# Kernel optimization log

Hardware: AMD Instinct MI355X
Metric: run time of the kernel (lower is better)

The kernel has to match this reference:

```python
import jax, jax.numpy as jnp
import numpy as np

NUM_EXPERTS = 8
TOP_K = 2
HIDDEN = 2048
INTER = 5632
NUM_TOKENS = 8192


def setup_inputs() -> dict:
    key = jax.random.key(0)
    ks = jax.random.split(key, 5)
    s_h = 1.0 / np.sqrt(HIDDEN)
    s_i = 1.0 / np.sqrt(INTER)
    return {
        "hidden_states": jax.random.normal(ks[0], (NUM_TOKENS, HIDDEN), jnp.float32),
        # router: ReplicatedLinear(hidden, num_experts, bias=False) -> weight [E, H]
        "w_router": jax.random.normal(ks[1], (NUM_EXPERTS, HIDDEN), jnp.float32) * s_h,
        # FusedMoE SiLU-gated MLP per expert: gate/up [E, H, I], down [E, I, H]
        "w_gate": jax.random.normal(ks[2], (NUM_EXPERTS, HIDDEN, INTER), jnp.float32) * s_h,
        "w_up": jax.random.normal(ks[3], (NUM_EXPERTS, HIDDEN, INTER), jnp.float32) * s_h,
        "w_down": jax.random.normal(ks[4], (NUM_EXPERTS, INTER, HIDDEN), jnp.float32) * s_i,
    }


def reference(hidden_states, w_router, w_gate, w_up, w_down):
    x = hidden_states  # [T, H]
    # Router linear (no bias)
    router_logits = x @ w_router.T  # [T, E]
    # FusedMoE topk: softmax over all experts, take top-k, renormalize=False
    probs = jax.nn.softmax(router_logits.astype(jnp.float32), axis=-1)
    topk_w, topk_idx = jax.lax.top_k(probs, TOP_K)  # [T, k]
    topk_w = topk_w.astype(x.dtype)

    out = jnp.zeros_like(x)
    for e in range(NUM_EXPERTS):
        # combine weight for tokens that routed to expert e (0 otherwise)
        w_e = jnp.sum(jnp.where(topk_idx == e, topk_w, 0.0), axis=-1)  # [T]
        h = jax.nn.silu(x @ w_gate[e]) * (x @ w_up[e])  # [T, I]
        out = out + (h @ w_down[e]) * w_e[:, None]
    return out
```

## Files before the change

### kernel.cpp

```cpp
#include <hip/hip_runtime.h>
#include <hip/hip_bf16.h>
#include <cstdint>

#define NTOK 8192
#define NEXP 8
#define HID  2048
#define INTR 5632
#define NT1  44
#define NT2  16
#define MT_MAX 32

#define XB_OFF 1048576u
#define WG_OFF 34603008u
#define WBYTES 184549376u
#define WU_OFF (WG_OFF + WBYTES)
#define WD_OFF (WU_OFF + WBYTES)
#define H_OFF  (WD_OFF + WBYTES)

typedef float f32x4  __attribute__((ext_vector_type(4)));
typedef short s16x8  __attribute__((ext_vector_type(8)));
typedef short s16x4  __attribute__((ext_vector_type(4)));

__device__ __forceinline__ short bfc(float f) {
  __hip_bfloat16 h = __float2bfloat16(f);
  return __builtin_bit_cast(short, h);
}
__device__ __forceinline__ s16x4 pk4(float4 a) {
  s16x4 v; v[0]=bfc(a.x); v[1]=bfc(a.y); v[2]=bfc(a.z); v[3]=bfc(a.w);
  return v;
}
__device__ __forceinline__ void gload16(const void* g, void* l) {
  __builtin_amdgcn_global_load_lds((const __attribute__((address_space(1))) void*)g,
                                   (__attribute__((address_space(3))) void*)l, 16, 0, 0);
}

#define DSR128(dst, addr, IMM) \
  asm volatile("ds_read_b128 %0, %1 offset:" IMM : "=v"(dst) : "v"(addr))
#define WAITLGKM(N) do { \
  asm volatile("s_waitcnt lgkmcnt(" #N ")" ::: "memory"); \
  __builtin_amdgcn_sched_barrier(0); } while (0)
#define WAITVM(N) do { \
  asm volatile("s_waitcnt vmcnt(" #N ")" ::: "memory"); \
  __builtin_amdgcn_sched_barrier(0); } while (0)

#define MFMA_BF16 __builtin_amdgcn_mfma_f32_16x16x32_bf16

__global__ __launch_bounds__(256, 4) void prep_kernel(
    const float* __restrict__ src, short* __restrict__ dst,
    int KT, int NP, int Nsrc) {
  __shared__ float tile[32 * 132];
  const int b = blockIdx.x;
  const int np = b % NP;
  const int kt = (b / NP) % KT;
  const int e  = b / (NP * KT);
  const int tid = threadIdx.x;
  const float* s = src + (size_t)e * KT * 32 * (size_t)Nsrc + (size_t)kt * 32 * Nsrc + np * 128;
#pragma unroll
  for (int i = 0; i < 4; i++) {
    const int idx = tid + i * 256;
    const int row = idx >> 5, c4 = idx & 31;
    float4 v = *(const float4*)(s + (size_t)row * Nsrc + c4 * 4);
    *(float4*)(tile + row * 132 + c4 * 4) = v;
  }
  __syncthreads();
  short* dbase = dst + ((size_t)(e * KT + kt) * (NP * 8) + np * 8) * 512;
#pragma unroll
  for (int i = 0; i < 2; i++) {
    const int c = tid + i * 256;
    const int lane = c & 63;
    const int nf = c >> 6;
    const int n = nf * 16 + (lane & 15);
    const int kb = (lane >> 4) * 8;
    s16x8 o;
#pragma unroll
    for (int j = 0; j < 8; j++) o[j] = bfc(tile[(kb + j) * 132 + n]);
    *(s16x8*)(dbase + (size_t)c * 8) = o;
  }
}

__global__ void router_kernel(const float* __restrict__ x, const float* __restrict__ wr,
                              int* __restrict__ cnt, int* __restrict__ lists,
                              float* __restrict__ wlists, __hip_bfloat16* __restrict__ xb) {
  const int wave = threadIdx.x >> 6;
  const int lane = threadIdx.x & 63;
  const int t = blockIdx.x * 4 + wave;
  if (t >= NTOK) return;
  float acc[NEXP];
#pragma unroll
  for (int e = 0; e < NEXP; e++) acc[e] = 0.f;
  const float* xrow = x + (size_t)t * HID;
  short* xbs = (short*)xb + (size_t)t * HID;
#pragma unroll
  for (int j = 0; j < HID / 256; j++) {
    const int k = j * 256 + lane * 4;
    float4 xv = *(const float4*)(xrow + k);
    *(s16x4*)(xbs + k) = pk4(xv);
#pragma unroll
    for (int e = 0; e < NEXP; e++) {
      float4 wv = *(const float4*)(wr + e * HID + k);
      acc[e] += xv.x * wv.x + xv.y * wv.y + xv.z * wv.z + xv.w * wv.w;
    }
  }
#pragma unroll
  for (int e = 0; e < NEXP; e++) {
    float v = acc[e];
    for (int off = 32; off; off >>= 1) v += __shfl_xor(v, off, 64);
    acc[e] = v;
  }
  if (lane == 0) {
    float m = acc[0];
#pragma unroll
    for (int e = 1; e < NEXP; e++) m = fmaxf(m, acc[e]);
    float p[NEXP], s = 0.f;
#pragma unroll
    for (int e = 0; e < NEXP; e++) { p[e] = __expf(acc[e] - m); s += p[e]; }
    const float inv = 1.f / s;
    int e1 = 0; float b1 = p[0];
#pragma unroll
    for (int e = 1; e < NEXP; e++) if (p[e] > b1) { b1 = p[e]; e1 = e; }
    int e2 = -1; float b2 = -1.f;
#pragma unroll
    for (int e = 0; e < NEXP; e++) if (e != e1 && p[e] > b2) { b2 = p[e]; e2 = e; }
    const int pos1 = atomicAdd(&cnt[e1], 1);
    lists[e1 * NTOK + pos1] = t; wlists[e1 * NTOK + pos1] = b1 * inv;
    const int pos2 = atomicAdd(&cnt[e2], 1);
    lists[e2 * NTOK + pos2] = t; wlists[e2 * NTOK + pos2] = b2 * inv;
  }
}

__global__ void offsets_kernel(const int* __restrict__ cnt, int* __restrict__ offs) {
  if (threadIdx.x == 0 && blockIdx.x == 0) {
    int o = 0;
#pragma unroll
    for (int e = 0; e < NEXP; e++) { offs[e] = o; o += cnt[e]; }
    offs[NEXP] = o;
  }
}

__global__ __launch_bounds__(512, 1) void gemm1_kernel(
    const __hip_bfloat16* __restrict__ xb, const short* __restrict__ wgb,
    const short* __restrict__ wub, const int* __restrict__ cnt,
    const int* __restrict__ offs, const int* __restrict__ lists,
    __hip_bfloat16* __restrict__ hbuf) {
  const int P = blockIdx.x;
  const int xcd = P & 7, slot = P >> 3;
  const int mt = slot & 31, jj = slot >> 5;
  const int g = jj * 8 + xcd;
  const int e = g / NT1, nt = g % NT1;
  const int count = cnt[e];
  if (mt * 256 >= count) return;
  const int n0 = nt * 128;
  const int lim = count - mt * 256;
  const int tid = threadIdx.x;
  const int w = tid >> 6, lane = tid & 63;
  const int wm = w >> 1, wn = w & 1;

  __shared__ short Lds[3 * 16384];
  short* rootA = &Lds[0];
  const uint32_t ldsbase = (uint32_t)(uintptr_t)rootA;

  const int* tl = lists + e * NTOK + mt * 256;
  const short* xbs = (const short*)xb;
  const short* srcA0; const short* srcA1;
  {
    const int r0 = (w * 2 + 0) * 16 + (lane & 15);
    const int r1 = (w * 2 + 1) * 16 + (lane & 15);
    const int t0 = tl[r0 < lim ? r0 : 0];
    const int t1 = tl[r1 < lim ? r1 : 0];
    srcA0 = xbs + (size_t)t0 * HID + (lane >> 4) * 8;
    srcA1 = xbs + (size_t)t1 * HID + (lane >> 4) * 8;
  }
  const short* srcBg = wgb + ((size_t)(e * 64) * 352 + nt * 8) * 512 + tid * 8;
  const short* srcBu = wub + ((size_t)(e * 64) * 352 + nt * 8) * 512 + tid * 8;

  const uint32_t roA = wm * 4096 + lane * 16;
  const uint32_t roB = 16384 + wn * 4096 + lane * 16;
  const uint32_t roU = 24576 + wn * 4096 + lane * 16;

  f32x4 accG[4][4], accU[4][4];
#pragma unroll
  for (int i = 0; i < 4; i++)
#pragma unroll
    for (int j = 0; j < 4; j++) {
      accG[i][j] = f32x4{0.f, 0.f, 0.f, 0.f};
      accU[i][j] = f32x4{0.f, 0.f, 0.f, 0.f};
    }

  uint32_t b0 = 0, b1 = 32768, b2 = 65536;

#define STG1(BOFF) do {                                                         \
    short* d = rootA + ((BOFF) >> 1);                                           \
    gload16(srcA0, d + (w * 2 + 0) * 512);                                      \
    gload16(srcA1, d + (w * 2 + 1) * 512);                                      \
    gload16(srcBg, d + 8192 + w * 512);                                         \
    gload16(srcBu, d + 12288 + w * 512);                                        \
    srcA0 += 32; srcA1 += 32; srcBg += 180224; srcBu += 180224; } while (0)

#define MMQ(NF)                                                                 \
  { __builtin_amdgcn_s_setprio(1);                                              \
    accG[0][NF] = MFMA_BF16(af[0], bgf[NF], accG[0][NF], 0, 0, 0);              \
    accU[0][NF] = MFMA_BF16(af[0], buf4[NF], accU[0][NF], 0, 0, 0);             \
    accG[1][NF] = MFMA_BF16(af[1], bgf[NF], accG[1][NF], 0, 0, 0);              \
    accU[1][NF] = MFMA_BF16(af[1], buf4[NF], accU[1][NF], 0, 0, 0);             \
    accG[2][NF] = MFMA_BF16(af[2], bgf[NF], accG[2][NF], 0, 0, 0);              \
    accU[2][NF] = MFMA_BF16(af[2], buf4[NF], accU[2][NF], 0, 0, 0);             \
    accG[3][NF] = MFMA_BF16(af[3], bgf[NF], accG[3][NF], 0, 0, 0);              \
    accU[3][NF] = MFMA_BF16(af[3], buf4[NF], accU[3][NF], 0, 0, 0);             \
    __builtin_amdgcn_s_setprio(0); }

#define G1_BODY(VM, DOSTG)                                                      \
  {                                                                             \
    WAITVM(VM);                                                                 \
    __builtin_amdgcn_s_barrier();                                               \
    const uint32_t rb = ldsbase + b0;                                           \
    s16x8 af[4], bgf[4], buf4[4];                                               \
    DSR128(bgf[0], rb + roB, "0");                                              \
    DSR128(buf4[0], rb + roU, "0");                                             \
    DSR128(af[0], rb + roA, "0");                                               \
    DSR128(af[1], rb + roA, "1024");                                            \
    DSR128(af[2], rb + roA, "2048");                                            \
    DSR128(af[3], rb + roA, "3072");                                            \
    DSR128(bgf[1], rb + roB, "1024");                                           \
    DSR128(buf4[1], rb + roU, "1024");                                          \
    DSR128(bgf[2], rb + roB, "2048");                                           \
    DSR128(buf4[2], rb + roU, "2048");                                          \
    DSR128(bgf[3], rb + roB, "3072");                                           \
    DSR128(buf4[3], rb + roU, "3072");                                          \
    if (DOSTG) { STG1(b2); }                                                    \
    WAITLGKM(6);                                                                \
    MMQ(0)                                                                      \
    WAITLGKM(4);                                                                \
    MMQ(1)                                                                      \
    WAITLGKM(2);                                                                \
    MMQ(2)                                                                      \
    WAITLGKM(0);                                                                \
    MMQ(3)                                                                      \
    const uint32_t rtmp = b0; b0 = b1; b1 = b2; b2 = rtmp;                      \
  }

  STG1(b0);
  STG1(b1);
  for (int t = 0; t < 62; ++t) G1_BODY(4, 1)
  G1_BODY(4, 0)
  G1_BODY(0, 0)
#undef G1_BODY
#undef MMQ
#undef STG1

  const int hrow0 = offs[e] + mt * 256;
#pragma unroll
  for (int mf = 0; mf < 4; mf++) {
#pragma unroll
    for (int reg = 0; reg < 4; reg++) {
      const int row = wm * 64 + mf * 16 + (lane >> 4) * 4 + reg;
      if (row < lim) {
        __hip_bfloat16* hp = hbuf + (size_t)(hrow0 + row) * INTR + n0 + wn * 64 + (lane & 15);
#pragma unroll
        for (int nf = 0; nf < 4; nf++) {
          const float gv = accG[mf][nf][reg];
          const float uv = accU[mf][nf][reg];
          const float h = (gv / (1.f + __expf(-gv))) * uv;
          hp[nf * 16] = __float2bfloat16(h);
        }
      }
    }
  }
}

__global__ __launch_bounds__(512, 1) void gemm2_kernel(
    const __hip_bfloat16* __restrict__ hbuf, const short* __restrict__ wdb,
    const int* __restrict__ cnt, const int* __restrict__ offs,
    const int* __restrict__ lists, const float* __restrict__ wlists,
    float* __restrict__ out) {
  const int P = blockIdx.x;
  const int xcd = P & 7, r = P >> 3;
  const int nt = r & 15, emq = r >> 4;
  const int gm = emq * 8 + xcd;
  const int e = gm >> 5, mt = gm & 31;
  const int count = cnt[e];
  if (mt * 256 >= count) return;
  const int n0 = nt * 128;
  const int lim = count - mt * 256;
  const int tid = threadIdx.x;
  const int w = tid >> 6, lane = tid & 63;
  const int wm = w >> 1, wn = w & 1;

  __shared__ short Lds[3 * 12288];
  short* rootA = &Lds[0];
  const uint32_t ldsbase = (uint32_t)(uintptr_t)rootA;

  const int sb = offs[e] + mt * 256;
  const short* hb = (const short*)hbuf;
  const short* srcA0; const short* srcA1;
  {
    int s0 = sb + (w * 2 + 0) * 16 + (lane & 15);
    int s1 = sb + (w * 2 + 1) * 16 + (lane & 15);
    if (s0 > 2 * NTOK - 1) s0 = 2 * NTOK - 1;
    if (s1 > 2 * NTOK - 1) s1 = 2 * NTOK - 1;
    srcA0 = hb + (size_t)s0 * INTR + (lane >> 4) * 8;
    srcA1 = hb + (size_t)s1 * INTR + (lane >> 4) * 8;
  }
  const short* srcB = wdb + ((size_t)(e * 176) * 128 + nt * 8) * 512 + tid * 8;

  const uint32_t roA = wm * 4096 + lane * 16;
  const uint32_t roB = 16384 + wn * 4096 + lane * 16;

  f32x4 acc[4][4];
#pragma unroll
  for (int i = 0; i < 4; i++)
#pragma unroll
    for (int j = 0; j < 4; j++) acc[i][j] = f32x4{0.f, 0.f, 0.f, 0.f};

  uint32_t b0 = 0, b1 = 24576, b2 = 49152;

#define STG2(BOFF) do {                                                         \
    short* d = rootA + ((BOFF) >> 1);                                           \
    gload16(srcA0, d + (w * 2 + 0) * 512);                                      \
    gload16(srcA1, d + (w * 2 + 1) * 512);                                      \
    gload16(srcB, d + 8192 + w * 512);                                          \
    srcA0 += 32; srcA1 += 32; srcB += 65536; } while (0)

#define MMQ2(NF)                                                                \
  { __builtin_amdgcn_s_setprio(1);                                              \
    acc[0][NF] = MFMA_BF16(af[0], bf[NF], acc[0][NF], 0, 0, 0);                 \
    acc[1][NF] = MFMA_BF16(af[1], bf[NF], acc[1][NF], 0, 0, 0);                 \
    acc[2][NF] = MFMA_BF16(af[2], bf[NF], acc[2][NF], 0, 0, 0);                 \
    acc[3][NF] = MFMA_BF16(af[3], bf[NF], acc[3][NF], 0, 0, 0);                 \
    __builtin_amdgcn_s_setprio(0); }

#define G2_BODY(VM, DOSTG)                                                      \
  {                                                                             \
    WAITVM(VM);                                                                 \
    __builtin_amdgcn_s_barrier();                                               \
    const uint32_t rb = ldsbase + b0;                                           \
    s16x8 af[4], bf[4];                                                         \
    DSR128(bf[0], rb + roB, "0");                                               \
    DSR128(af[0], rb + roA, "0");                                               \
    DSR128(af[1], rb + roA, "1024");                                            \
    DSR128(af[2], rb + roA, "2048");                                            \
    DSR128(af[3], rb + roA, "3072");                                            \
    DSR128(bf[1], rb + roB, "1024");                                            \
    DSR128(bf[2], rb + roB, "2048");                                            \
    DSR128(bf[3], rb + roB, "3072");                                            \
    if (DOSTG) { STG2(b2); }                                                    \
    WAITLGKM(3);                                                                \
    MMQ2(0)                                                                     \
    WAITLGKM(2);                                                                \
    MMQ2(1)                                                                     \
    WAITLGKM(1);                                                                \
    MMQ2(2)                                                                     \
    WAITLGKM(0);                                                                \
    MMQ2(3)                                                                     \
    const uint32_t rtmp = b0; b0 = b1; b1 = b2; b2 = rtmp;                      \
  }

  STG2(b0);
  STG2(b1);
  for (int t = 0; t < 174; ++t) G2_BODY(3, 1)
  G2_BODY(3, 0)
  G2_BODY(0, 0)
#undef G2_BODY
#undef MMQ2
#undef STG2

  const int* tle = lists + e * NTOK + mt * 256;
  const float* wle = wlists + e * NTOK + mt * 256;
#pragma unroll
  for (int mf = 0; mf < 4; mf++) {
#pragma unroll
    for (int reg = 0; reg < 4; reg++) {
      const int row = wm * 64 + mf * 16 + (lane >> 4) * 4 + reg;
      if (row < lim) {
        const int tok = tle[row];
        const float wt = wle[row];
        float* op = out + (size_t)tok * HID + n0 + wn * 64 + (lane & 15);
#pragma unroll
        for (int nf = 0; nf < 4; nf++)
          atomicAdd(op + nf * 16, acc[mf][nf][reg] * wt);
      }
    }
  }
}

extern "C" void kernel_launch(void* const* d_in, const int* in_sizes, int n_in,
                              void* d_out, int out_size, void* d_ws, size_t ws_size,
                              hipStream_t stream) {
  const float* x  = (const float*)d_in[0];
  const float* wr = (const float*)d_in[1];
  const float* wg = (const float*)d_in[2];
  const float* wu = (const float*)d_in[3];
  const float* wd = (const float*)d_in[4];
  float* out = (float*)d_out;
  char* ws = (char*)d_ws;

  int* cnt    = (int*)ws;
  int* offs   = cnt + 8;
  int* lists  = cnt + 32;
  float* wlists = (float*)(lists + NEXP * NTOK);
  __hip_bfloat16* xbf = (__hip_bfloat16*)(ws + XB_OFF);
  short* wgb = (short*)(ws + WG_OFF);
  short* wub = (short*)(ws + WU_OFF);
  short* wdb = (short*)(ws + WD_OFF);
  __hip_bfloat16* hbuf = (__hip_bfloat16*)(ws + H_OFF);

  hipMemsetAsync(cnt, 0, 32 * sizeof(int), stream);
  hipMemsetAsync(out, 0, (size_t)NTOK * HID * sizeof(float), stream);

  router_kernel<<<NTOK / 4, 256, 0, stream>>>(x, wr, cnt, lists, wlists, xbf);
  offsets_kernel<<<1, 64, 0, stream>>>(cnt, offs);
  prep_kernel<<<NEXP * 64 * 44, 256, 0, stream>>>(wg, wgb, 64, 44, INTR);
  prep_kernel<<<NEXP * 64 * 44, 256, 0, stream>>>(wu, wub, 64, 44, INTR);
  prep_kernel<<<NEXP * 176 * 16, 256, 0, stream>>>(wd, wdb, 176, 16, HID);
  gemm1_kernel<<<NEXP * NT1 * MT_MAX, 512, 0, stream>>>(xbf, wgb, wub, cnt, offs, lists, hbuf);
  gemm2_kernel<<<NEXP * NT2 * MT_MAX, 512, 0, stream>>>(hbuf, wdb, cnt, offs, lists, wlists, out);
}
```

Before: 1.964 ms.

## Restructure MoE pipeline with padded slots, pre-gathered fragment inputs, and atomic-free combine

Tokens are assigned padded per-expert slots, and a gather kernel writes the routed activations as bf16 in MFMA fragment order. GEMM1 now uses 256-thread blocks with 128-row tiles and double buffering, and writes h in fragment layout so GEMM2 can load it directly. GEMM2 writes bf16 per-slot partial outputs instead of doing float atomics, and a combine kernel applies the routing weights. The down-projection weights reuse the gate buffer after GEMM1, which saves workspace. The cost is extra kernels, bf16 rounding of partial outputs, and extra padded-row work.

```diff
diff --git a/kernel.cpp b/kernel.cpp
--- a/kernel.cpp
+++ b/kernel.cpp
@@ -8,14 +8,19 @@
 #define INTR 5632
 #define NT1  44
 #define NT2  16
-#define MT_MAX 32
-
-#define XB_OFF 1048576u
-#define WG_OFF 34603008u
-#define WBYTES 184549376u
-#define WU_OFF (WG_OFF + WBYTES)
-#define WD_OFF (WU_OFF + WBYTES)
-#define H_OFF  (WD_OFF + WBYTES)
+
+#define TCNT_OFF    4096u
+#define SLOT_OFF    65536u
+#define T2S_OFF     262144u
+#define W2_OFF      393216u
+#define LISTS_OFF   524288u
+#define WL_OFF      786432u
+#define WG_OFF      2097152u
+#define WBYTES      184549376u
+#define WU_OFF      (WG_OFF + WBYTES)
+#define HF_OFF      (WU_OFF + WBYTES)
+#define HFBYTES     207618048u
+#define XG_OFF      (HF_OFF + HFBYTES)
 
 typedef float f32x4  __attribute__((ext_vector_type(4)));
 typedef short s16x8  __attribute__((ext_vector_type(8)));
@@ -25,8 +30,14 @@
   __hip_bfloat16 h = __float2bfloat16(f);
   return __builtin_bit_cast(short, h);
 }
-__device__ __forceinline__ s16x4 pk4(float4 a) {
-  s16x4 v; v[0]=bfc(a.x); v[1]=bfc(a.y); v[2]=bfc(a.z); v[3]=bfc(a.w);
+__device__ __forceinline__ float b2f(short s) {
+  unsigned u = ((unsigned)(unsigned short)s) << 16;
+  return __builtin_bit_cast(float, u);
+}
+__device__ __forceinline__ s16x8 pk8(float4 a, float4 b) {
+  s16x8 v;
+  v[0]=bfc(a.x); v[1]=bfc(a.y); v[2]=bfc(a.z); v[3]=bfc(a.w);
+  v[4]=bfc(b.x); v[5]=bfc(b.y); v[6]=bfc(b.z); v[7]=bfc(b.w);
   return v;
 }
 __device__ __forceinline__ void gload16(const void* g, void* l) {
@@ -80,7 +91,7 @@
 
 __global__ void router_kernel(const float* __restrict__ x, const float* __restrict__ wr,
                               int* __restrict__ cnt, int* __restrict__ lists,
-                              float* __restrict__ wlists, __hip_bfloat16* __restrict__ xb) {
+                              float* __restrict__ wlists) {
   const int wave = threadIdx.x >> 6;
   const int lane = threadIdx.x & 63;
   const int t = blockIdx.x * 4 + wave;
@@ -89,12 +100,10 @@
 #pragma unroll
   for (int e = 0; e < NEXP; e++) acc[e] = 0.f;
   const float* xrow = x + (size_t)t * HID;
-  short* xbs = (short*)xb + (size_t)t * HID;
 #pragma unroll
   for (int j = 0; j < HID / 256; j++) {
     const int k = j * 256 + lane * 4;
     float4 xv = *(const float4*)(xrow + k);
-    *(s16x4*)(xbs + k) = pk4(xv);
 #pragma unroll
     for (int e = 0; e < NEXP; e++) {
       float4 wv = *(const float4*)(wr + e * HID + k);
@@ -128,54 +137,72 @@
   }
 }
 
-__global__ void offsets_kernel(const int* __restrict__ cnt, int* __restrict__ offs) {
+__global__ void offsets_kernel(const int* __restrict__ cnt, int* __restrict__ poffs) {
   if (threadIdx.x == 0 && blockIdx.x == 0) {
     int o = 0;
 #pragma unroll
-    for (int e = 0; e < NEXP; e++) { offs[e] = o; o += cnt[e]; }
-    offs[NEXP] = o;
-  }
-}
-
-__global__ __launch_bounds__(512, 1) void gemm1_kernel(
-    const __hip_bfloat16* __restrict__ xb, const short* __restrict__ wgb,
+    for (int e = 0; e < NEXP; e++) { poffs[e] = o; o += ((cnt[e] + 255) >> 8) << 8; }
+    poffs[NEXP] = o;
+  }
+}
+
+__global__ void slotmap_kernel(const int* __restrict__ cnt, const int* __restrict__ poffs,
+                               const int* __restrict__ lists, const float* __restrict__ wlists,
+                               int* __restrict__ slotlist, int* __restrict__ tcnt,
+                               int* __restrict__ tok2slot, float* __restrict__ w2) {
+  const int e = blockIdx.x;
+  const int c = cnt[e], base = poffs[e];
+  for (int pos = threadIdx.x; pos < c; pos += blockDim.x) {
+    const int tok = lists[e * NTOK + pos];
+    const int slot = base + pos;
+    slotlist[slot] = tok;
+    const int j = atomicAdd(&tcnt[tok], 1);
+    tok2slot[tok * 2 + j] = slot;
+    w2[tok * 2 + j] = wlists[e * NTOK + pos];
+  }
+}
+
+__global__ __launch_bounds__(256, 4) void gather_kernel(
+    const float* __restrict__ x, const int* __restrict__ slotlist,
+    short* __restrict__ xg) {
+  const int c = blockIdx.x * 256 + threadIdx.x;
+  const int cl = c & 63;
+  const int fragid = c >> 6;
+  const int f = fragid & 15;
+  const int kt = (fragid >> 4) & 63;
+  const int gmt = fragid >> 10;
+  const int tok = slotlist[gmt * 256 + f * 16 + (cl & 15)];
+  const float* s = x + (size_t)tok * HID + kt * 32 + (cl >> 4) * 8;
+  float4 a = *(const float4*)s, b = *(const float4*)(s + 4);
+  *(s16x8*)(xg + (size_t)c * 8) = pk8(a, b);
+}
+
+__global__ __launch_bounds__(256, 2) void gemm1_kernel(
+    const short* __restrict__ xg, const short* __restrict__ wgb,
     const short* __restrict__ wub, const int* __restrict__ cnt,
-    const int* __restrict__ offs, const int* __restrict__ lists,
-    __hip_bfloat16* __restrict__ hbuf) {
+    const int* __restrict__ poffs, short* __restrict__ hfrag) {
   const int P = blockIdx.x;
   const int xcd = P & 7, slot = P >> 3;
-  const int mt = slot & 31, jj = slot >> 5;
+  const int mt = slot & 63, jj = slot >> 6;
   const int g = jj * 8 + xcd;
   const int e = g / NT1, nt = g % NT1;
-  const int count = cnt[e];
-  if (mt * 256 >= count) return;
-  const int n0 = nt * 128;
-  const int lim = count - mt * 256;
+  if (mt * 128 >= cnt[e]) return;
+  const int gmt = (poffs[e] >> 8) + (mt >> 1);
+  const int fhalf = (mt & 1) * 8;
   const int tid = threadIdx.x;
   const int w = tid >> 6, lane = tid & 63;
   const int wm = w >> 1, wn = w & 1;
 
-  __shared__ short Lds[3 * 16384];
-  short* rootA = &Lds[0];
-  const uint32_t ldsbase = (uint32_t)(uintptr_t)rootA;
-
-  const int* tl = lists + e * NTOK + mt * 256;
-  const short* xbs = (const short*)xb;
-  const short* srcA0; const short* srcA1;
-  {
-    const int r0 = (w * 2 + 0) * 16 + (lane & 15);
-    const int r1 = (w * 2 + 1) * 16 + (lane & 15);
-    const int t0 = tl[r0 < lim ? r0 : 0];
-    const int t1 = tl[r1 < lim ? r1 : 0];
-    srcA0 = xbs + (size_t)t0 * HID + (lane >> 4) * 8;
-    srcA1 = xbs + (size_t)t1 * HID + (lane >> 4) * 8;
-  }
-  const short* srcBg = wgb + ((size_t)(e * 64) * 352 + nt * 8) * 512 + tid * 8;
-  const short* srcBu = wub + ((size_t)(e * 64) * 352 + nt * 8) * 512 + tid * 8;
+  __shared__ __align__(16) short Lds[2 * 12288];
+  const uint32_t ldsbase = (uint32_t)(uintptr_t)&Lds[0];
+
+  const short* srcA  = xg  + (((size_t)gmt * 64) * 16 + fhalf + w * 2) * 512 + lane * 8;
+  const short* srcBg = wgb + (((size_t)e * 64) * 352 + nt * 8 + w * 2) * 512 + lane * 8;
+  const short* srcBu = wub + (((size_t)e * 64) * 352 + nt * 8 + w * 2) * 512 + lane * 8;
 
   const uint32_t roA = wm * 4096 + lane * 16;
-  const uint32_t roB = 16384 + wn * 4096 + lane * 16;
-  const uint32_t roU = 24576 + wn * 4096 + lane * 16;
+  const uint32_t roB = 8192 + wn * 4096 + lane * 16;
+  const uint32_t roU = 16384 + wn * 4096 + lane * 16;
 
   f32x4 accG[4][4], accU[4][4];
 #pragma unroll
@@ -186,15 +213,17 @@
       accU[i][j] = f32x4{0.f, 0.f, 0.f, 0.f};
     }
 
-  uint32_t b0 = 0, b1 = 32768, b2 = 65536;
+  uint32_t cur = 0;
 
 #define STG1(BOFF) do {                                                         \
-    short* d = rootA + ((BOFF) >> 1);                                           \
-    gload16(srcA0, d + (w * 2 + 0) * 512);                                      \
-    gload16(srcA1, d + (w * 2 + 1) * 512);                                      \
-    gload16(srcBg, d + 8192 + w * 512);                                         \
-    gload16(srcBu, d + 12288 + w * 512);                                        \
-    srcA0 += 32; srcA1 += 32; srcBg += 180224; srcBu += 180224; } while (0)
+    short* d = (short*)Lds + ((BOFF) >> 1);                                     \
+    gload16(srcA,        d + w * 1024);                                         \
+    gload16(srcA + 512,  d + w * 1024 + 512);                                   \
+    gload16(srcBg,       d + 4096 + w * 1024);                                  \
+    gload16(srcBg + 512, d + 4096 + w * 1024 + 512);                            \
+    gload16(srcBu,       d + 8192 + w * 1024);                                  \
+    gload16(srcBu + 512, d + 8192 + w * 1024 + 512);                            \
+    srcA += 8192; srcBg += 180224; srcBu += 180224; } while (0)
 
 #define MMQ(NF)                                                                 \
   { __builtin_amdgcn_s_setprio(1);                                              \
@@ -208,11 +237,11 @@
     accU[3][NF] = MFMA_BF16(af[3], buf4[NF], accU[3][NF], 0, 0, 0);             \
     __builtin_amdgcn_s_setprio(0); }
 
-#define G1_BODY(VM, DOSTG)                                                      \
+#define G1_BODY(DOSTG)                                                          \
   {                                                                             \
-    WAITVM(VM);                                                                 \
+    WAITVM(0);                                                                  \
     __builtin_amdgcn_s_barrier();                                               \
-    const uint32_t rb = ldsbase + b0;                                           \
+    const uint32_t rb = ldsbase + cur;                                          \
     s16x8 af[4], bgf[4], buf4[4];                                               \
     DSR128(bgf[0], rb + roB, "0");                                              \
     DSR128(buf4[0], rb + roU, "0");                                             \
@@ -226,7 +255,7 @@
     DSR128(buf4[2], rb + roU, "2048");                                          \
     DSR128(bgf[3], rb + roB, "3072");                                           \
     DSR128(buf4[3], rb + roU, "3072");                                          \
-    if (DOSTG) { STG1(b2); }                                                    \
+    if (DOSTG) { STG1(cur ^ 24576); }                                           \
     WAITLGKM(6);                                                                \
     MMQ(0)                                                                      \
     WAITLGKM(4);                                                                \
@@ -235,72 +264,66 @@
     MMQ(2)                                                                      \
     WAITLGKM(0);                                                                \
     MMQ(3)                                                                      \
-    const uint32_t rtmp = b0; b0 = b1; b1 = b2; b2 = rtmp;                      \
-  }
-
-  STG1(b0);
-  STG1(b1);
-  for (int t = 0; t < 62; ++t) G1_BODY(4, 1)
-  G1_BODY(4, 0)
-  G1_BODY(0, 0)
+    cur ^= 24576;                                                               \
+  }
+
+  STG1(0);
+  for (int t = 0; t < 63; ++t) G1_BODY(1)
+  G1_BODY(0)
 #undef G1_BODY
 #undef MMQ
 #undef STG1
 
-  const int hrow0 = offs[e] + mt * 256;
-#pragma unroll
-  for (int mf = 0; mf < 4; mf++) {
+  short* tr = (short*)Lds;
+  __syncthreads();
+#pragma unroll
+  for (int mf = 0; mf < 4; mf++)
 #pragma unroll
     for (int reg = 0; reg < 4; reg++) {
       const int row = wm * 64 + mf * 16 + (lane >> 4) * 4 + reg;
-      if (row < lim) {
-        __hip_bfloat16* hp = hbuf + (size_t)(hrow0 + row) * INTR + n0 + wn * 64 + (lane & 15);
-#pragma unroll
-        for (int nf = 0; nf < 4; nf++) {
-          const float gv = accG[mf][nf][reg];
-          const float uv = accU[mf][nf][reg];
-          const float h = (gv / (1.f + __expf(-gv))) * uv;
-          hp[nf * 16] = __float2bfloat16(h);
-        }
+#pragma unroll
+      for (int nf = 0; nf < 4; nf++) {
+        const int col = wn * 64 + nf * 16 + (lane & 15);
+        const float gv = accG[mf][nf][reg];
+        const float uv = accU[mf][nf][reg];
+        tr[row * 136 + col] = bfc((gv / (1.f + __expf(-gv))) * uv);
       }
     }
-  }
-}
-
-__global__ __launch_bounds__(512, 1) void gemm2_kernel(
-    const __hip_bfloat16* __restrict__ hbuf, const short* __restrict__ wdb,
-    const int* __restrict__ cnt, const int* __restrict__ offs,
-    const int* __restrict__ lists, const float* __restrict__ wlists,
-    float* __restrict__ out) {
+  __syncthreads();
+  short* hb = hfrag + (((size_t)gmt * 176 + nt * 4) * 16 + fhalf) * 512;
+#pragma unroll
+  for (int i = 0; i < 8; i++) {
+    const int c = tid + i * 256;
+    const int cl = c & 63;
+    const int f7 = (c >> 6) & 7;
+    const int ktl = c >> 9;
+    const int rr = f7 * 16 + (cl & 15);
+    s16x8 v = *(const s16x8*)(tr + rr * 136 + ktl * 32 + (cl >> 4) * 8);
+    *(s16x8*)(hb + ((size_t)ktl * 16 + f7) * 512 + cl * 8) = v;
+  }
+}
+
+__global__ __launch_bounds__(512, 4) void gemm2_kernel(
+    const short* __restrict__ hfrag, const short* __restrict__ wdb,
+    const int* __restrict__ cnt, const int* __restrict__ poffs,
+    __hip_bfloat16* __restrict__ pout) {
   const int P = blockIdx.x;
   const int xcd = P & 7, r = P >> 3;
   const int nt = r & 15, emq = r >> 4;
   const int gm = emq * 8 + xcd;
   const int e = gm >> 5, mt = gm & 31;
-  const int count = cnt[e];
-  if (mt * 256 >= count) return;
+  if (mt * 256 >= cnt[e]) return;
+  const int gmt = (poffs[e] >> 8) + mt;
   const int n0 = nt * 128;
-  const int lim = count - mt * 256;
   const int tid = threadIdx.x;
   const int w = tid >> 6, lane = tid & 63;
   const int wm = w >> 1, wn = w & 1;
 
-  __shared__ short Lds[3 * 12288];
-  short* rootA = &Lds[0];
-  const uint32_t ldsbase = (uint32_t)(uintptr_t)rootA;
-
-  const int sb = offs[e] + mt * 256;
-  const short* hb = (const short*)hbuf;
-  const short* srcA0; const short* srcA1;
-  {
-    int s0 = sb + (w * 2 + 0) * 16 + (lane & 15);
-    int s1 = sb + (w * 2 + 1) * 16 + (lane & 15);
-    if (s0 > 2 * NTOK - 1) s0 = 2 * NTOK - 1;
-    if (s1 > 2 * NTOK - 1) s1 = 2 * NTOK - 1;
-    srcA0 = hb + (size_t)s0 * INTR + (lane >> 4) * 8;
-    srcA1 = hb + (size_t)s1 * INTR + (lane >> 4) * 8;
-  }
-  const short* srcB = wdb + ((size_t)(e * 176) * 128 + nt * 8) * 512 + tid * 8;
+  __shared__ __align__(16) short Lds[2 * 12288];
+  const uint32_t ldsbase = (uint32_t)(uintptr_t)&Lds[0];
+
+  const short* srcA = hfrag + (((size_t)gmt * 176) * 16 + w * 2) * 512 + lane * 8;
+  const short* srcB = wdb + (((size_t)e * 176) * 128 + nt * 8) * 512 + tid * 8;
 
   const uint32_t roA = wm * 4096 + lane * 16;
   const uint32_t roB = 16384 + wn * 4096 + lane * 16;
@@ -311,14 +334,14 @@
 #pragma unroll
     for (int j = 0; j < 4; j++) acc[i][j] = f32x4{0.f, 0.f, 0.f, 0.f};
 
-  uint32_t b0 = 0, b1 = 24576, b2 = 49152;
+  uint32_t cur = 0;
 
 #define STG2(BOFF) do {                                                         \
-    short* d = rootA + ((BOFF) >> 1);                                           \
-    gload16(srcA0, d + (w * 2 + 0) * 512);                                      \
-    gload16(srcA1, d + (w * 2 + 1) * 512);                                      \
-    gload16(srcB, d + 8192 + w * 512);                                          \
-    srcA0 += 32; srcA1 += 32; srcB += 65536; } while (0)
+    short* d = (short*)Lds + ((BOFF) >> 1);                                     \
+    gload16(srcA,       d + w * 1024);                                          \
+    gload16(srcA + 512, d + w * 1024 + 512);                                    \
+    gload16(srcB,       d + 8192 + w * 512);                                    \
+    srcA += 8192; srcB += 65536; } while (0)
 
 #define MMQ2(NF)                                                                \
   { __builtin_amdgcn_s_setprio(1);                                              \
@@ -328,11 +351,11 @@
     acc[3][NF] = MFMA_BF16(af[3], bf[NF], acc[3][NF], 0, 0, 0);                 \
     __builtin_amdgcn_s_setprio(0); }
 
-#define G2_BODY(VM, DOSTG)                                                      \
+#define G2_BODY(DOSTG)                                                          \
   {                                                                             \
-    WAITVM(VM);                                                                 \
+    WAITVM(0);                                                                  \
     __builtin_amdgcn_s_barrier();                                               \
-    const uint32_t rb = ldsbase + b0;                                           \
+    const uint32_t rb = ldsbase + cur;                                          \
     s16x8 af[4], bf[4];                                                         \
     DSR128(bf[0], rb + roB, "0");                                               \
     DSR128(af[0], rb + roA, "0");                                               \
@@ -342,7 +365,7 @@
     DSR128(bf[1], rb + roB, "1024");                                            \
     DSR128(bf[2], rb + roB, "2048");                                            \
     DSR128(bf[3], rb + roB, "3072");                                            \
-    if (DOSTG) { STG2(b2); }                                                    \
+    if (DOSTG) { STG2(cur ^ 24576); }                                           \
     WAITLGKM(3);                                                                \
     MMQ2(0)                                                                     \
     WAITLGKM(2);                                                                \
@@ -351,35 +374,53 @@
     MMQ2(2)                                                                     \
     WAITLGKM(0);                                                                \
     MMQ2(3)                                                                     \
-    const uint32_t rtmp = b0; b0 = b1; b1 = b2; b2 = rtmp;                      \
-  }
-
-  STG2(b0);
-  STG2(b1);
-  for (int t = 0; t < 174; ++t) G2_BODY(3, 1)
-  G2_BODY(3, 0)
-  G2_BODY(0, 0)
+    cur ^= 24576;                                                               \
+  }
+
+  STG2(0);
+  for (int t = 0; t < 175; ++t) G2_BODY(1)
+  G2_BODY(0)
 #undef G2_BODY
 #undef MMQ2
 #undef STG2
 
-  const int* tle = lists + e * NTOK + mt * 256;
-  const float* wle = wlists + e * NTOK + mt * 256;
+  const int slotb = poffs[e] + mt * 256;
 #pragma unroll
   for (int mf = 0; mf < 4; mf++) {
 #pragma unroll
     for (int reg = 0; reg < 4; reg++) {
       const int row = wm * 64 + mf * 16 + (lane >> 4) * 4 + reg;
-      if (row < lim) {
-        const int tok = tle[row];
-        const float wt = wle[row];
-        float* op = out + (size_t)tok * HID + n0 + wn * 64 + (lane & 15);
-#pragma unroll
-        for (int nf = 0; nf < 4; nf++)
-          atomicAdd(op + nf * 16, acc[mf][nf][reg] * wt);
-      }
+      __hip_bfloat16* op = pout + (size_t)(slotb + row) * HID + n0 + wn * 64 + (lane & 15);
+#pragma unroll
+      for (int nf = 0; nf < 4; nf++)
+        op[nf * 16] = __float2bfloat16(acc[mf][nf][reg]);
     }
   }
+}
+
+__global__ __launch_bounds__(256, 8) void combine_kernel(
+    const __hip_bfloat16* __restrict__ pout, const int* __restrict__ tok2slot,
+    const float* __restrict__ w2, float* __restrict__ out) {
+  const int t = blockIdx.x;
+  const int s0 = tok2slot[2 * t], s1 = tok2slot[2 * t + 1];
+  const float w0 = w2[2 * t], w1 = w2[2 * t + 1];
+  const short* p0 = (const short*)pout + (size_t)s0 * HID;
+  const short* p1 = (const short*)pout + (size_t)s1 * HID;
+  float* o = out + (size_t)t * HID;
+  const int i = threadIdx.x;
+  s16x8 a = *(const s16x8*)(p0 + i * 8);
+  s16x8 b = *(const s16x8*)(p1 + i * 8);
+  float4 r0, r1;
+  r0.x = w0 * b2f(a[0]) + w1 * b2f(b[0]);
+  r0.y = w0 * b2f(a[1]) + w1 * b2f(b[1]);
+  r0.z = w0 * b2f(a[2]) + w1 * b2f(b[2]);
+  r0.w = w0 * b2f(a[3]) + w1 * b2f(b[3]);
+  r1.x = w0 * b2f(a[4]) + w1 * b2f(b[4]);
+  r1.y = w0 * b2f(a[5]) + w1 * b2f(b[5]);
+  r1.z = w0 * b2f(a[6]) + w1 * b2f(b[6]);
+  r1.w = w0 * b2f(a[7]) + w1 * b2f(b[7]);
+  *(float4*)(o + i * 8) = r0;
+  *(float4*)(o + i * 8 + 4) = r1;
 }
 
 extern "C" void kernel_launch(void* const* d_in, const int* in_sizes, int n_in,
@@ -393,24 +434,33 @@
   float* out = (float*)d_out;
   char* ws = (char*)d_ws;
 
-  int* cnt    = (int*)ws;
-  int* offs   = cnt + 8;
-  int* lists  = cnt + 32;
-  float* wlists = (float*)(lists + NEXP * NTOK);
-  __hip_bfloat16* xbf = (__hip_bfloat16*)(ws + XB_OFF);
-  short* wgb = (short*)(ws + WG_OFF);
-  short* wub = (short*)(ws + WU_OFF);
-  short* wdb = (short*)(ws + WD_OFF);
-  __hip_bfloat16* hbuf = (__hip_bfloat16*)(ws + H_OFF);
-
-  hipMemsetAsync(cnt, 0, 32 * sizeof(int), stream);
-  hipMemsetAsync(out, 0, (size_t)NTOK * HID * sizeof(float), stream);
-
-  router_kernel<<<NTOK / 4, 256, 0, stream>>>(x, wr, cnt, lists, wlists, xbf);
-  offsets_kernel<<<1, 64, 0, stream>>>(cnt, offs);
+  int* cnt      = (int*)ws;
+  int* poffs    = (int*)(ws + 64);
+  int* tcnt     = (int*)(ws + TCNT_OFF);
+  int* slotlist = (int*)(ws + SLOT_OFF);
+  int* tok2slot = (int*)(ws + T2S_OFF);
+  float* w2     = (float*)(ws + W2_OFF);
+  int* lists    = (int*)(ws + LISTS_OFF);
+  float* wlists = (float*)(ws + WL_OFF);
+  short* wgb    = (short*)(ws + WG_OFF);
+  short* wub    = (short*)(ws + WU_OFF);
+  short* wdb    = (short*)(ws + WG_OFF);
+  short* hfrag  = (short*)(ws + HF_OFF);
+  short* xg     = (short*)(ws + XG_OFF);
+  __hip_bfloat16* pout = (__hip_bfloat16*)(ws + XG_OFF);
+
+  hipMemsetAsync(ws, 0, 256, stream);
+  hipMemsetAsync(ws + TCNT_OFF, 0, 32768, stream);
+  hipMemsetAsync(ws + SLOT_OFF, 0, 73728, stream);
+
+  router_kernel<<<NTOK / 4, 256, 0, stream>>>(x, wr, cnt, lists, wlists);
+  offsets_kernel<<<1, 64, 0, stream>>>(cnt, poffs);
+  slotmap_kernel<<<NEXP, 256, 0, stream>>>(cnt, poffs, lists, wlists, slotlist, tcnt, tok2slot, w2);
+  gather_kernel<<<18432, 256, 0, stream>>>(x, slotlist, xg);
   prep_kernel<<<NEXP * 64 * 44, 256, 0, stream>>>(wg, wgb, 64, 44, INTR);
   prep_kernel<<<NEXP * 64 * 44, 256, 0, stream>>>(wu, wub, 64, 44, INTR);
+  gemm1_kernel<<<8 * 64 * NT1, 256, 0, stream>>>(xg, wgb, wub, cnt, poffs, hfrag);
   prep_kernel<<<NEXP * 176 * 16, 256, 0, stream>>>(wd, wdb, 176, 16, HID);
-  gemm1_kernel<<<NEXP * NT1 * MT_MAX, 512, 0, stream>>>(xbf, wgb, wub, cnt, offs, lists, hbuf);
-  gemm2_kernel<<<NEXP * NT2 * MT_MAX, 512, 0, stream>>>(hbuf, wdb, cnt, offs, lists, wlists, out);
-}
+  gemm2_kernel<<<8 * 16 * 32, 512, 0, stream>>>(hfrag, wdb, cnt, poffs, pout);
+  combine_kernel<<<NTOK, 256, 0, stream>>>(pout, tok2slot, w2, out);
+}
```

Measured after the change: 1.752 ms. 10.8% less time.
